# Kernel tuning notes

Measured on AMD Instinct MI355X. Metric: run time of the kernel, lower is better.

## Reference

```python
import jax, jax.numpy as jnp
import numpy as np

BN_EPS = 1e-5

def _bn_relu(x, gamma, beta):
    # BatchNorm1d in training mode: batch stats over (B, N) per channel
    mean = jnp.mean(x, axis=(0, 1), keepdims=True)
    var = jnp.var(x, axis=(0, 1), keepdims=True)
    return jax.nn.relu((x - mean) * jax.lax.rsqrt(var + BN_EPS) * gamma + beta)

def setup_inputs() -> dict:
    key = jax.random.key(0)
    ks = jax.random.split(key, 8)
    B, N, S, C1, C2 = 8, 8192, 2048, 128, 256
    return {
        'xyz1': jax.random.normal(ks[0], (B, N, 3), jnp.float32),
        'xyz2': jax.random.normal(ks[1], (B, S, 3), jnp.float32),
        'points1': jax.random.normal(ks[2], (B, N, C1), jnp.float32),
        'points2': jax.random.normal(ks[3], (B, S, C2), jnp.float32),
        'w0': jax.random.normal(ks[4], (256, C1 + C2), jnp.float32) * 0.02,
        'b0': jnp.zeros((256,), jnp.float32),
        'g0': jnp.ones((256,), jnp.float32),
        'be0': jnp.zeros((256,), jnp.float32),
        'w1': jax.random.normal(ks[5], (128, 256), jnp.float32) * 0.02,
        'b1': jnp.zeros((128,), jnp.float32),
        'g1': jnp.ones((128,), jnp.float32),
        'be1': jnp.zeros((128,), jnp.float32),
    }

def reference(xyz1, xyz2, points1, points2, w0, b0, g0, be0, w1, b1, g1, be1):
    # squared pairwise distances [B, N, S]
    sq = (jnp.sum(xyz1 * xyz1, -1)[:, :, None]
          - 2.0 * jnp.einsum('bnc,bmc->bnm', xyz1, xyz2)
          + jnp.sum(xyz2 * xyz2, -1)[:, None, :])
    neg_d, idx = jax.lax.top_k(-sq, 3)          # smallest 3 distances
    dist = -neg_d                               # [B, N, 3]
    recip = 1.0 / (dist + 1e-8)
    weight = recip / jnp.sum(recip, -1, keepdims=True)
    gathered = jax.vmap(lambda p, i: p[i])(points2, idx)   # [B, N, 3, C2]
    interp = jnp.sum(gathered * weight[..., None], axis=2)  # [B, N, C2]
    x = jnp.concatenate([points1, interp], axis=-1)         # [B, N, C1+C2]
    x = _bn_relu(jnp.einsum('bnc,oc->bno', x, w0) + b0, g0, be0)
    x = _bn_relu(jnp.einsum('bnc,oc->bno', x, w1) + b1, g1, be1)
    return x
```

## Files before the change

kernel.cpp:

```cpp
#include <hip/hip_runtime.h>

#define B_  8
#define N_  8192
#define S_  2048
#define C1_ 128
#define C2_ 256
#define KA_ 384
#define H0_ 256
#define H1_ 128
#define R_  (B_ * N_)

typedef __bf16 bf16;
typedef __attribute__((ext_vector_type(2))) __bf16 bf16x2;
typedef __attribute__((ext_vector_type(4))) __bf16 bf16x4;
typedef __attribute__((ext_vector_type(8))) __bf16 bf16x8;
typedef __attribute__((ext_vector_type(4))) float f32x4;

__device__ __forceinline__ void gload_lds16(const void* g, void* l) {
    __builtin_amdgcn_global_load_lds(
        (const __attribute__((address_space(1))) void*)g,
        (__attribute__((address_space(3))) void*)l, 16, 0, 0);
}

__global__ void zero_kernel(float* __restrict__ p, int n) {
    int i = blockIdx.x * 256 + threadIdx.x;
    if (i < n) p[i] = 0.f;
}

__global__ __launch_bounds__(256) void cvt_kernel(const float* __restrict__ src,
                                                  bf16* __restrict__ dst, int n4) {
    int i = blockIdx.x * 256 + threadIdx.x;
    if (i < n4) {
        float4 v = *(const float4*)(src + (size_t)i * 4);
        bf16x4 o = { (bf16)v.x, (bf16)v.y, (bf16)v.z, (bf16)v.w };
        *(bf16x4*)(dst + (size_t)i * 4) = o;
    }
}

__global__ __launch_bounds__(256) void top3_kernel(
    const float* __restrict__ xyz1, const float* __restrict__ xyz2,
    int* __restrict__ out_idx, float* __restrict__ out_w)
{
    __shared__ float4 sc[S_];
    __shared__ float  md[64][4][3];
    __shared__ int    mi[64][4][3];

    int b = blockIdx.x >> 7;
    int ntile = blockIdx.x & 127;
    const float* src = xyz2 + (size_t)b * S_ * 3;
    for (int i = threadIdx.x; i < S_; i += 256) {
        float x = src[i * 3 + 0], y = src[i * 3 + 1], z = src[i * 3 + 2];
        float4 c; c.x = x; c.y = y; c.z = z; c.w = x * x + y * y + z * z;
        sc[i] = c;
    }
    __syncthreads();

    const int q  = threadIdx.x >> 2;
    const int sp = threadIdx.x & 3;
    const size_t row = (size_t)b * N_ + ntile * 64 + q;
    const float ax = -2.f * xyz1[row * 3 + 0];
    const float ay = -2.f * xyz1[row * 3 + 1];
    const float az = -2.f * xyz1[row * 3 + 2];

    float m0 = 1e30f, m1 = 1e30f, m2 = 1e30f;
    int   j0 = 0, j1 = 0, j2 = 0;

    #pragma unroll 4
    for (int i = 0; i < S_ / 4; ++i) {
        int s = i * 4 + sp;
        float4 c = sc[s];
        float m = fmaf(ax, c.x, fmaf(ay, c.y, fmaf(az, c.z, c.w)));
        if (m < m2) {
            if (m < m1) {
                m2 = m1; j2 = j1;
                if (m < m0) { m1 = m0; j1 = j0; m0 = m; j0 = s; }
                else        { m1 = m;  j1 = s; }
            } else { m2 = m; j2 = s; }
        }
    }
    md[q][sp][0] = m0; md[q][sp][1] = m1; md[q][sp][2] = m2;
    mi[q][sp][0] = j0; mi[q][sp][1] = j1; mi[q][sp][2] = j2;
    __syncthreads();

    if (threadIdx.x < 64) {
        int qq = threadIdx.x;
        float d0 = md[qq][0][0], d1 = md[qq][0][1], d2 = md[qq][0][2];
        int   i0 = mi[qq][0][0], i1 = mi[qq][0][1], i2 = mi[qq][0][2];
        #pragma unroll
        for (int p = 1; p < 4; ++p) {
            #pragma unroll
            for (int j = 0; j < 3; ++j) {
                float d = md[qq][p][j]; int s = mi[qq][p][j];
                bool lt2 = (d < d2) || (d == d2 && s < i2);
                if (lt2) {
                    bool lt1 = (d < d1) || (d == d1 && s < i1);
                    if (lt1) {
                        d2 = d1; i2 = i1;
                        bool lt0 = (d < d0) || (d == d0 && s < i0);
                        if (lt0) { d1 = d0; i1 = i0; d0 = d; i0 = s; }
                        else     { d1 = d;  i1 = s; }
                    } else { d2 = d; i2 = s; }
                }
            }
        }
        size_t orow = (size_t)b * N_ + ntile * 64 + qq;
        float px = xyz1[orow * 3 + 0], py = xyz1[orow * 3 + 1], pz = xyz1[orow * 3 + 2];
        float pp = px * px + py * py + pz * pz;
        float r0 = 1.f / (d0 + pp + 1e-8f);
        float r1 = 1.f / (d1 + pp + 1e-8f);
        float r2 = 1.f / (d2 + pp + 1e-8f);
        float inv = 1.f / (r0 + r1 + r2);
        out_idx[orow * 3 + 0] = i0; out_idx[orow * 3 + 1] = i1; out_idx[orow * 3 + 2] = i2;
        out_w[orow * 3 + 0] = r0 * inv; out_w[orow * 3 + 1] = r1 * inv; out_w[orow * 3 + 2] = r2 * inv;
    }
}

__global__ __launch_bounds__(256) void interp_kernel(
    const float* __restrict__ points1, const float* __restrict__ points2,
    const int* __restrict__ idx3, const float* __restrict__ w3,
    bf16* __restrict__ Abf)
{
    int t = threadIdx.x;
    size_t row = (size_t)blockIdx.x * 4 + (t >> 6);
    int lane = t & 63;
    int b = (int)(row >> 13);
    const float* p2 = points2 + (size_t)b * S_ * C2_;
    int ia = idx3[row * 3 + 0], ib = idx3[row * 3 + 1], ic = idx3[row * 3 + 2];
    float wa = w3[row * 3 + 0], wb = w3[row * 3 + 1], wc = w3[row * 3 + 2];
    float4 va = *(const float4*)(p2 + (size_t)ia * C2_ + lane * 4);
    float4 vb = *(const float4*)(p2 + (size_t)ib * C2_ + lane * 4);
    float4 vc = *(const float4*)(p2 + (size_t)ic * C2_ + lane * 4);
    bf16x4 o = { (bf16)(wa * va.x + wb * vb.x + wc * vc.x),
                 (bf16)(wa * va.y + wb * vb.y + wc * vc.y),
                 (bf16)(wa * va.z + wb * vb.z + wc * vc.z),
                 (bf16)(wa * va.w + wb * vb.w + wc * vc.w) };
    *(bf16x4*)(Abf + row * KA_ + C1_ + lane * 4) = o;

    float2 p = *(const float2*)(points1 + row * C1_ + lane * 2);
    bf16x2 po = { (bf16)p.x, (bf16)p.y };
    *(bf16x2*)(Abf + row * KA_ + lane * 2) = po;
}

template<int K, int OT, bool OUTBF>
__global__ __launch_bounds__(256) void mfma_gemm_kernel(
    const bf16* __restrict__ A, const bf16* __restrict__ Wt, void* __restrict__ Cout,
    float* __restrict__ sums, float* __restrict__ sumsq)
{
    __shared__ bf16 As[128 * 32];
    __shared__ bf16 Bs[128 * 32];
    __shared__ float csum[128], csumsq[128];
    const int tid = threadIdx.x;
    const int lane = tid & 63, wave = tid >> 6;
    const int wr = wave >> 1, wc = wave & 1;
    const int r0 = blockIdx.x * 128, o0 = blockIdx.y * 128;

    f32x4 acc[4][4] = {};

    const int l15 = lane & 15, g = lane >> 4;
    const int slot = g ^ ((l15 >> 1) & 3);
    int a_off[4], b_off[4];
    #pragma unroll
    for (int m = 0; m < 4; ++m) a_off[m] = (wr * 64 + m * 16 + l15) * 32 + slot * 8;
    #pragma unroll
    for (int n = 0; n < 4; ++n) b_off[n] = (wc * 64 + n * 16 + l15) * 32 + slot * 8;

    const int c0 = tid, c1 = tid + 256;
    const int ar0 = c0 >> 2, ar1 = c1 >> 2;
    const int kb0 = ((c0 & 3) ^ ((ar0 >> 1) & 3)) * 8;
    const int kb1 = ((c1 & 3) ^ ((ar1 >> 1) & 3)) * 8;

    if (tid < 128) { csum[tid] = 0.f; csumsq[tid] = 0.f; }

    for (int k0 = 0; k0 < K; k0 += 32) {
        __syncthreads();
        gload_lds16(A  + (size_t)(r0 + ar0) * K + k0 + kb0, &As[c0 * 8]);
        gload_lds16(A  + (size_t)(r0 + ar1) * K + k0 + kb1, &As[c1 * 8]);
        gload_lds16(Wt + (size_t)(o0 + ar0) * K + k0 + kb0, &Bs[c0 * 8]);
        gload_lds16(Wt + (size_t)(o0 + ar1) * K + k0 + kb1, &Bs[c1 * 8]);
        __syncthreads();
        bf16x8 af[4], bfr[4];
        #pragma unroll
        for (int m = 0; m < 4; ++m) af[m]  = *(const bf16x8*)&As[a_off[m]];
        #pragma unroll
        for (int n = 0; n < 4; ++n) bfr[n] = *(const bf16x8*)&Bs[b_off[n]];
        #pragma unroll
        for (int m = 0; m < 4; ++m)
            #pragma unroll
            for (int n = 0; n < 4; ++n)
                acc[m][n] = __builtin_amdgcn_mfma_f32_16x16x32_bf16(af[m], bfr[n], acc[m][n], 0, 0, 0);
    }

    const int crow = r0 + wr * 64 + g * 4;
    const int ccol = o0 + wc * 64 + l15;
    #pragma unroll
    for (int m = 0; m < 4; ++m)
        #pragma unroll
        for (int n = 0; n < 4; ++n)
            #pragma unroll
            for (int j = 0; j < 4; ++j) {
                size_t off = (size_t)(crow + m * 16 + j) * OT + ccol + n * 16;
                if (OUTBF) ((bf16*)Cout)[off] = (bf16)acc[m][n][j];
                else       ((float*)Cout)[off] = acc[m][n][j];
            }

    #pragma unroll
    for (int n = 0; n < 4; ++n) {
        float s = 0.f, q = 0.f;
        #pragma unroll
        for (int m = 0; m < 4; ++m)
            #pragma unroll
            for (int j = 0; j < 4; ++j) {
                float v = acc[m][n][j];
                s += v; q = fmaf(v, v, q);
            }
        int col = wc * 64 + n * 16 + l15;
        atomicAdd(&csum[col], s);
        atomicAdd(&csumsq[col], q);
    }
    __syncthreads();
    if (tid < 128) {
        atomicAdd(&sums[o0 + tid], csum[tid]);
        atomicAdd(&sumsq[o0 + tid], csumsq[tid]);
    }
}

__global__ __launch_bounds__(256) void mfma_gemm2_kernel(
    const bf16* __restrict__ Ahp, const bf16* __restrict__ Wt,
    const float* __restrict__ scale, const float* __restrict__ shift,
    float* __restrict__ Cout, float* __restrict__ sums, float* __restrict__ sumsq)
{
    constexpr int K = H0_, OT = H1_;
    __shared__ bf16 As[128 * 32];
    __shared__ bf16 Bs[128 * 32];
    __shared__ float csum[128], csumsq[128];
    const int tid = threadIdx.x;
    const int lane = tid & 63, wave = tid >> 6;
    const int wr = wave >> 1, wc = wave & 1;
    const int r0 = blockIdx.x * 128, o0 = blockIdx.y * 128;

    f32x4 acc[4][4] = {};

    const int l15 = lane & 15, g = lane >> 4;
    const int slot = g ^ ((l15 >> 1) & 3);
    int a_off[4], b_off[4];
    #pragma unroll
    for (int m = 0; m < 4; ++m) a_off[m] = (wr * 64 + m * 16 + l15) * 32 + slot * 8;
    #pragma unroll
    for (int n = 0; n < 4; ++n) b_off[n] = (wc * 64 + n * 16 + l15) * 32 + slot * 8;

    const int c0 = tid, c1 = tid + 256;
    const int ar0 = c0 >> 2, ar1 = c1 >> 2;
    const int kb0 = ((c0 & 3) ^ ((ar0 >> 1) & 3)) * 8;
    const int kb1 = ((c1 & 3) ^ ((ar1 >> 1) & 3)) * 8;

    if (tid < 128) { csum[tid] = 0.f; csumsq[tid] = 0.f; }

    for (int k0 = 0; k0 < K; k0 += 32) {
        bf16x8 va0 = *(const bf16x8*)(Ahp + (size_t)(r0 + ar0) * K + k0 + kb0);
        bf16x8 va1 = *(const bf16x8*)(Ahp + (size_t)(r0 + ar1) * K + k0 + kb1);
        float s0a[8], h0a[8], s1a[8], h1a[8];
        *(float4*)&s0a[0] = *(const float4*)(scale + k0 + kb0);
        *(float4*)&s0a[4] = *(const float4*)(scale + k0 + kb0 + 4);
        *(float4*)&h0a[0] = *(const float4*)(shift + k0 + kb0);
        *(float4*)&h0a[4] = *(const float4*)(shift + k0 + kb0 + 4);
        *(float4*)&s1a[0] = *(const float4*)(scale + k0 + kb1);
        *(float4*)&s1a[4] = *(const float4*)(scale + k0 + kb1 + 4);
        *(float4*)&h1a[0] = *(const float4*)(shift + k0 + kb1);
        *(float4*)&h1a[4] = *(const float4*)(shift + k0 + kb1 + 4);
        bf16x8 ra0, ra1;
        #pragma unroll
        for (int j = 0; j < 8; ++j) {
            float f0 = fmaxf(0.f, fmaf((float)va0[j], s0a[j], h0a[j]));
            float f1 = fmaxf(0.f, fmaf((float)va1[j], s1a[j], h1a[j]));
            ra0[j] = (bf16)f0; ra1[j] = (bf16)f1;
        }
        __syncthreads();
        gload_lds16(Wt + (size_t)(o0 + ar0) * K + k0 + kb0, &Bs[c0 * 8]);
        gload_lds16(Wt + (size_t)(o0 + ar1) * K + k0 + kb1, &Bs[c1 * 8]);
        *(bf16x8*)&As[c0 * 8] = ra0;
        *(bf16x8*)&As[c1 * 8] = ra1;
        __syncthreads();
        bf16x8 af[4], bfr[4];
        #pragma unroll
        for (int m = 0; m < 4; ++m) af[m]  = *(const bf16x8*)&As[a_off[m]];
        #pragma unroll
        for (int n = 0; n < 4; ++n) bfr[n] = *(const bf16x8*)&Bs[b_off[n]];
        #pragma unroll
        for (int m = 0; m < 4; ++m)
            #pragma unroll
            for (int n = 0; n < 4; ++n)
                acc[m][n] = __builtin_amdgcn_mfma_f32_16x16x32_bf16(af[m], bfr[n], acc[m][n], 0, 0, 0);
    }

    const int crow = r0 + wr * 64 + g * 4;
    const int ccol = o0 + wc * 64 + l15;
    #pragma unroll
    for (int m = 0; m < 4; ++m)
        #pragma unroll
        for (int n = 0; n < 4; ++n)
            #pragma unroll
            for (int j = 0; j < 4; ++j)
                ((float*)Cout)[(size_t)(crow + m * 16 + j) * OT + ccol + n * 16] = acc[m][n][j];

    #pragma unroll
    for (int n = 0; n < 4; ++n) {
        float s = 0.f, q = 0.f;
        #pragma unroll
        for (int m = 0; m < 4; ++m)
            #pragma unroll
            for (int j = 0; j < 4; ++j) {
                float v = acc[m][n][j];
                s += v; q = fmaf(v, v, q);
            }
        int col = wc * 64 + n * 16 + l15;
        atomicAdd(&csum[col], s);
        atomicAdd(&csumsq[col], q);
    }
    __syncthreads();
    if (tid < 128) {
        atomicAdd(&sums[o0 + tid], csum[tid]);
        atomicAdd(&sumsq[o0 + tid], csumsq[tid]);
    }
}

__global__ void finalize_kernel(const float* __restrict__ sums, const float* __restrict__ sumsq,
                                const float* __restrict__ g, const float* __restrict__ be,
                                float* __restrict__ scale, float* __restrict__ shift, float invR)
{
    int c = threadIdx.x;
    float mean = sums[c] * invR;
    float var = sumsq[c] * invR - mean * mean;
    float s = g[c] * rsqrtf(var + 1e-5f);
    scale[c] = s;
    shift[c] = be[c] - mean * s;
}

__global__ __launch_bounds__(256) void bnrelu_kernel(float* __restrict__ X,
                                                     const float* __restrict__ scale,
                                                     const float* __restrict__ shift)
{
    size_t i = (size_t)blockIdx.x * 256 + threadIdx.x;
    float4 v = *(float4*)(X + i * 4);
    int c = (int)((i * 4) & (H1_ - 1));
    v.x = fmaxf(0.f, v.x * scale[c + 0] + shift[c + 0]);
    v.y = fmaxf(0.f, v.y * scale[c + 1] + shift[c + 1]);
    v.z = fmaxf(0.f, v.z * scale[c + 2] + shift[c + 2]);
    v.w = fmaxf(0.f, v.w * scale[c + 3] + shift[c + 3]);
    *(float4*)(X + i * 4) = v;
}

extern "C" void kernel_launch(void* const* d_in, const int* in_sizes, int n_in,
                              void* d_out, int out_size, void* d_ws, size_t ws_size,
                              hipStream_t stream)
{
    const float* xyz1    = (const float*)d_in[0];
    const float* xyz2    = (const float*)d_in[1];
    const float* points1 = (const float*)d_in[2];
    const float* points2 = (const float*)d_in[3];
    const float* w0  = (const float*)d_in[4];
    const float* g0  = (const float*)d_in[6];
    const float* be0 = (const float*)d_in[7];
    const float* w1  = (const float*)d_in[8];
    const float* g1  = (const float*)d_in[10];
    const float* be1 = (const float*)d_in[11];
    float* out = (float*)d_out;
    char* ws = (char*)d_ws;

    bf16* Abf     = (bf16*)(ws);
    bf16* hpre_bf = (bf16*)(ws + 50331648);
    bf16* Wbf0    = (bf16*)(ws + 117440512);
    bf16* Wbf1    = (bf16*)(ws + 117637120);
    int*  idx3    = (int*) (ws + 117702656);
    float* w3     = (float*)(ws + 118489088);
    float* stats  = (float*)(ws + 119275520);
    float* sums0 = stats,        *sumsq0 = stats + 256;
    float* sums1 = stats + 512,  *sumsq1 = stats + 640;
    float* scale0 = stats + 768,  *shift0 = stats + 1024;
    float* scale1 = stats + 1280, *shift1 = stats + 1408;

    zero_kernel<<<3, 256, 0, stream>>>(stats, 768);
    cvt_kernel<<<96, 256, 0, stream>>>(w0, Wbf0, H0_ * KA_ / 4);
    cvt_kernel<<<32, 256, 0, stream>>>(w1, Wbf1, H1_ * H0_ / 4);
    top3_kernel<<<B_ * (N_ / 64), 256, 0, stream>>>(xyz1, xyz2, idx3, w3);
    interp_kernel<<<R_ / 4, 256, 0, stream>>>(points1, points2, idx3, w3, Abf);

    mfma_gemm_kernel<KA_, H0_, true><<<dim3(R_ / 128, 2), 256, 0, stream>>>(
        Abf, Wbf0, hpre_bf, sums0, sumsq0);
    finalize_kernel<<<1, 256, 0, stream>>>(sums0, sumsq0, g0, be0, scale0, shift0, 1.f / R_);

    mfma_gemm2_kernel<<<dim3(R_ / 128, 1), 256, 0, stream>>>(
        hpre_bf, Wbf1, scale0, shift0, out, sums1, sumsq1);
    finalize_kernel<<<1, 128, 0, stream>>>(sums1, sumsq1, g1, be1, scale1, shift1, 1.f / R_);
    bnrelu_kernel<<<R_ * H1_ / 4 / 256, 256, 0, stream>>>(out, scale1, shift1);
}
```

Baseline: 183.9 us.

## Fuse top3 with interpolation and fold BN finalize into consumer kernels

Merges the zero and weight-conversion launches into one prep kernel. Fuses top-3 search with the interpolation gather so indices and weights stay in shared memory instead of a global round trip. Computes the BN scale and shift inside gemm2 and bnrelu, removing both finalize launches, and makes bnrelu process four float4s per thread. Launch overhead and small global traffic drop, but the interpolation phase now runs inside the top3 grid with only 1024 blocks, which may reduce gather parallelism.

```diff
diff --git a/kernel.cpp b/kernel.cpp
--- a/kernel.cpp
+++ b/kernel.cpp
@@ -22,28 +22,39 @@
         (__attribute__((address_space(3))) void*)l, 16, 0, 0);
 }
 
-__global__ void zero_kernel(float* __restrict__ p, int n) {
-    int i = blockIdx.x * 256 + threadIdx.x;
-    if (i < n) p[i] = 0.f;
-}
-
-__global__ __launch_bounds__(256) void cvt_kernel(const float* __restrict__ src,
-                                                  bf16* __restrict__ dst, int n4) {
-    int i = blockIdx.x * 256 + threadIdx.x;
-    if (i < n4) {
-        float4 v = *(const float4*)(src + (size_t)i * 4);
+__global__ __launch_bounds__(256) void prep_kernel(const float* __restrict__ w0,
+                                                   const float* __restrict__ w1,
+                                                   bf16* __restrict__ Wbf0,
+                                                   bf16* __restrict__ Wbf1,
+                                                   float* __restrict__ stats)
+{
+    int blk = blockIdx.x, tid = threadIdx.x;
+    if (blk < 96) {
+        int i = blk * 256 + tid;
+        float4 v = *(const float4*)(w0 + (size_t)i * 4);
         bf16x4 o = { (bf16)v.x, (bf16)v.y, (bf16)v.z, (bf16)v.w };
-        *(bf16x4*)(dst + (size_t)i * 4) = o;
-    }
-}
-
-__global__ __launch_bounds__(256) void top3_kernel(
+        *(bf16x4*)(Wbf0 + (size_t)i * 4) = o;
+    } else if (blk < 128) {
+        int i = (blk - 96) * 256 + tid;
+        float4 v = *(const float4*)(w1 + (size_t)i * 4);
+        bf16x4 o = { (bf16)v.x, (bf16)v.y, (bf16)v.z, (bf16)v.w };
+        *(bf16x4*)(Wbf1 + (size_t)i * 4) = o;
+    } else {
+        #pragma unroll
+        for (int k = 0; k < 3; ++k) stats[k * 256 + tid] = 0.f;
+    }
+}
+
+__global__ __launch_bounds__(256) void top3_interp_kernel(
     const float* __restrict__ xyz1, const float* __restrict__ xyz2,
-    int* __restrict__ out_idx, float* __restrict__ out_w)
+    const float* __restrict__ points1, const float* __restrict__ points2,
+    bf16* __restrict__ Abf)
 {
     __shared__ float4 sc[S_];
     __shared__ float  md[64][4][3];
     __shared__ int    mi[64][4][3];
+    __shared__ int    sidx[64][3];
+    __shared__ float  sw[64][3];
 
     int b = blockIdx.x >> 7;
     int ntile = blockIdx.x & 127;
@@ -110,35 +121,31 @@
         float r1 = 1.f / (d1 + pp + 1e-8f);
         float r2 = 1.f / (d2 + pp + 1e-8f);
         float inv = 1.f / (r0 + r1 + r2);
-        out_idx[orow * 3 + 0] = i0; out_idx[orow * 3 + 1] = i1; out_idx[orow * 3 + 2] = i2;
-        out_w[orow * 3 + 0] = r0 * inv; out_w[orow * 3 + 1] = r1 * inv; out_w[orow * 3 + 2] = r2 * inv;
-    }
-}
-
-__global__ __launch_bounds__(256) void interp_kernel(
-    const float* __restrict__ points1, const float* __restrict__ points2,
-    const int* __restrict__ idx3, const float* __restrict__ w3,
-    bf16* __restrict__ Abf)
-{
-    int t = threadIdx.x;
-    size_t row = (size_t)blockIdx.x * 4 + (t >> 6);
-    int lane = t & 63;
-    int b = (int)(row >> 13);
+        sidx[qq][0] = i0; sidx[qq][1] = i1; sidx[qq][2] = i2;
+        sw[qq][0] = r0 * inv; sw[qq][1] = r1 * inv; sw[qq][2] = r2 * inv;
+    }
+    __syncthreads();
+
+    const int wv = threadIdx.x >> 6, ln = threadIdx.x & 63;
+    const size_t rowbase = (size_t)b * N_ + ntile * 64;
     const float* p2 = points2 + (size_t)b * S_ * C2_;
-    int ia = idx3[row * 3 + 0], ib = idx3[row * 3 + 1], ic = idx3[row * 3 + 2];
-    float wa = w3[row * 3 + 0], wb = w3[row * 3 + 1], wc = w3[row * 3 + 2];
-    float4 va = *(const float4*)(p2 + (size_t)ia * C2_ + lane * 4);
-    float4 vb = *(const float4*)(p2 + (size_t)ib * C2_ + lane * 4);
-    float4 vc = *(const float4*)(p2 + (size_t)ic * C2_ + lane * 4);
-    bf16x4 o = { (bf16)(wa * va.x + wb * vb.x + wc * vc.x),
-                 (bf16)(wa * va.y + wb * vb.y + wc * vc.y),
-                 (bf16)(wa * va.z + wb * vb.z + wc * vc.z),
-                 (bf16)(wa * va.w + wb * vb.w + wc * vc.w) };
-    *(bf16x4*)(Abf + row * KA_ + C1_ + lane * 4) = o;
-
-    float2 p = *(const float2*)(points1 + row * C1_ + lane * 2);
-    bf16x2 po = { (bf16)p.x, (bf16)p.y };
-    *(bf16x2*)(Abf + row * KA_ + lane * 2) = po;
+    for (int r = wv; r < 64; r += 4) {
+        size_t orow = rowbase + r;
+        int ia = sidx[r][0], ib = sidx[r][1], ic = sidx[r][2];
+        float wa = sw[r][0], wb = sw[r][1], wc = sw[r][2];
+        float4 va = *(const float4*)(p2 + (size_t)ia * C2_ + ln * 4);
+        float4 vb = *(const float4*)(p2 + (size_t)ib * C2_ + ln * 4);
+        float4 vc = *(const float4*)(p2 + (size_t)ic * C2_ + ln * 4);
+        bf16x4 o = { (bf16)(wa * va.x + wb * vb.x + wc * vc.x),
+                     (bf16)(wa * va.y + wb * vb.y + wc * vc.y),
+                     (bf16)(wa * va.z + wb * vb.z + wc * vc.z),
+                     (bf16)(wa * va.w + wb * vb.w + wc * vc.w) };
+        *(bf16x4*)(Abf + orow * KA_ + C1_ + ln * 4) = o;
+
+        float2 p = *(const float2*)(points1 + orow * C1_ + ln * 2);
+        bf16x2 po = { (bf16)p.x, (bf16)p.y };
+        *(bf16x2*)(Abf + orow * KA_ + ln * 2) = po;
+    }
 }
 
 template<int K, int OT, bool OUTBF>
@@ -226,18 +233,31 @@
 
 __global__ __launch_bounds__(256) void mfma_gemm2_kernel(
     const bf16* __restrict__ Ahp, const bf16* __restrict__ Wt,
-    const float* __restrict__ scale, const float* __restrict__ shift,
+    const float* __restrict__ sums0, const float* __restrict__ sumsq0,
+    const float* __restrict__ g0, const float* __restrict__ be0,
     float* __restrict__ Cout, float* __restrict__ sums, float* __restrict__ sumsq)
 {
     constexpr int K = H0_, OT = H1_;
     __shared__ bf16 As[128 * 32];
     __shared__ bf16 Bs[128 * 32];
     __shared__ float csum[128], csumsq[128];
+    __shared__ float sscale[256], sshift[256];
     const int tid = threadIdx.x;
     const int lane = tid & 63, wave = tid >> 6;
     const int wr = wave >> 1, wc = wave & 1;
     const int r0 = blockIdx.x * 128, o0 = blockIdx.y * 128;
 
+    {
+        const float invR = 1.f / (float)R_;
+        float mean = sums0[tid] * invR;
+        float var = sumsq0[tid] * invR - mean * mean;
+        float sv = g0[tid] * rsqrtf(var + 1e-5f);
+        sscale[tid] = sv;
+        sshift[tid] = be0[tid] - mean * sv;
+    }
+    if (tid < 128) { csum[tid] = 0.f; csumsq[tid] = 0.f; }
+    __syncthreads();
+
     f32x4 acc[4][4] = {};
 
     const int l15 = lane & 15, g = lane >> 4;
@@ -253,20 +273,18 @@
     const int kb0 = ((c0 & 3) ^ ((ar0 >> 1) & 3)) * 8;
     const int kb1 = ((c1 & 3) ^ ((ar1 >> 1) & 3)) * 8;
 
-    if (tid < 128) { csum[tid] = 0.f; csumsq[tid] = 0.f; }
-
     for (int k0 = 0; k0 < K; k0 += 32) {
         bf16x8 va0 = *(const bf16x8*)(Ahp + (size_t)(r0 + ar0) * K + k0 + kb0);
         bf16x8 va1 = *(const bf16x8*)(Ahp + (size_t)(r0 + ar1) * K + k0 + kb1);
         float s0a[8], h0a[8], s1a[8], h1a[8];
-        *(float4*)&s0a[0] = *(const float4*)(scale + k0 + kb0);
-        *(float4*)&s0a[4] = *(const float4*)(scale + k0 + kb0 + 4);
-        *(float4*)&h0a[0] = *(const float4*)(shift + k0 + kb0);
-        *(float4*)&h0a[4] = *(const float4*)(shift + k0 + kb0 + 4);
-        *(float4*)&s1a[0] = *(const float4*)(scale + k0 + kb1);
-        *(float4*)&s1a[4] = *(const float4*)(scale + k0 + kb1 + 4);
-        *(float4*)&h1a[0] = *(const float4*)(shift + k0 + kb1);
-        *(float4*)&h1a[4] = *(const float4*)(shift + k0 + kb1 + 4);
+        *(float4*)&s0a[0] = *(const float4*)(&sscale[k0 + kb0]);
+        *(float4*)&s0a[4] = *(const float4*)(&sscale[k0 + kb0 + 4]);
+        *(float4*)&h0a[0] = *(const float4*)(&sshift[k0 + kb0]);
+        *(float4*)&h0a[4] = *(const float4*)(&sshift[k0 + kb0 + 4]);
+        *(float4*)&s1a[0] = *(const float4*)(&sscale[k0 + kb1]);
+        *(float4*)&s1a[4] = *(const float4*)(&sscale[k0 + kb1 + 4]);
+        *(float4*)&h1a[0] = *(const float4*)(&sshift[k0 + kb1]);
+        *(float4*)&h1a[4] = *(const float4*)(&sshift[k0 + kb1 + 4]);
         bf16x8 ra0, ra1;
         #pragma unroll
         for (int j = 0; j < 8; ++j) {
@@ -323,30 +341,34 @@
     }
 }
 
-__global__ void finalize_kernel(const float* __restrict__ sums, const float* __restrict__ sumsq,
-                                const float* __restrict__ g, const float* __restrict__ be,
-                                float* __restrict__ scale, float* __restrict__ shift, float invR)
-{
-    int c = threadIdx.x;
-    float mean = sums[c] * invR;
-    float var = sumsq[c] * invR - mean * mean;
-    float s = g[c] * rsqrtf(var + 1e-5f);
-    scale[c] = s;
-    shift[c] = be[c] - mean * s;
-}
-
-__global__ __launch_bounds__(256) void bnrelu_kernel(float* __restrict__ X,
-                                                     const float* __restrict__ scale,
-                                                     const float* __restrict__ shift)
-{
-    size_t i = (size_t)blockIdx.x * 256 + threadIdx.x;
-    float4 v = *(float4*)(X + i * 4);
-    int c = (int)((i * 4) & (H1_ - 1));
-    v.x = fmaxf(0.f, v.x * scale[c + 0] + shift[c + 0]);
-    v.y = fmaxf(0.f, v.y * scale[c + 1] + shift[c + 1]);
-    v.z = fmaxf(0.f, v.z * scale[c + 2] + shift[c + 2]);
-    v.w = fmaxf(0.f, v.w * scale[c + 3] + shift[c + 3]);
-    *(float4*)(X + i * 4) = v;
+__global__ __launch_bounds__(256) void bnrelu_kernel(
+    float* __restrict__ X, const float* __restrict__ sums1,
+    const float* __restrict__ sumsq1, const float* __restrict__ g1,
+    const float* __restrict__ be1)
+{
+    __shared__ float ss[128], sh[128];
+    int tid = threadIdx.x;
+    if (tid < 128) {
+        const float invR = 1.f / (float)R_;
+        float mean = sums1[tid] * invR;
+        float var = sumsq1[tid] * invR - mean * mean;
+        float sv = g1[tid] * rsqrtf(var + 1e-5f);
+        ss[tid] = sv;
+        sh[tid] = be1[tid] - mean * sv;
+    }
+    __syncthreads();
+
+    #pragma unroll
+    for (int it = 0; it < 4; ++it) {
+        size_t i = (size_t)it * 524288 + (size_t)blockIdx.x * 256 + tid;
+        int c = ((int)i & 31) * 4;
+        float4 v = *(float4*)(X + i * 4);
+        v.x = fmaxf(0.f, v.x * ss[c + 0] + sh[c + 0]);
+        v.y = fmaxf(0.f, v.y * ss[c + 1] + sh[c + 1]);
+        v.z = fmaxf(0.f, v.z * ss[c + 2] + sh[c + 2]);
+        v.w = fmaxf(0.f, v.w * ss[c + 3] + sh[c + 3]);
+        *(float4*)(X + i * 4) = v;
+    }
 }
 
 extern "C" void kernel_launch(void* const* d_in, const int* in_sizes, int n_in,
@@ -370,26 +392,18 @@
     bf16* hpre_bf = (bf16*)(ws + 50331648);
     bf16* Wbf0    = (bf16*)(ws + 117440512);
     bf16* Wbf1    = (bf16*)(ws + 117637120);
-    int*  idx3    = (int*) (ws + 117702656);
-    float* w3     = (float*)(ws + 118489088);
     float* stats  = (float*)(ws + 119275520);
     float* sums0 = stats,        *sumsq0 = stats + 256;
     float* sums1 = stats + 512,  *sumsq1 = stats + 640;
-    float* scale0 = stats + 768,  *shift0 = stats + 1024;
-    float* scale1 = stats + 1280, *shift1 = stats + 1408;
-
-    zero_kernel<<<3, 256, 0, stream>>>(stats, 768);
-    cvt_kernel<<<96, 256, 0, stream>>>(w0, Wbf0, H0_ * KA_ / 4);
-    cvt_kernel<<<32, 256, 0, stream>>>(w1, Wbf1, H1_ * H0_ / 4);
-    top3_kernel<<<B_ * (N_ / 64), 256, 0, stream>>>(xyz1, xyz2, idx3, w3);
-    interp_kernel<<<R_ / 4, 256, 0, stream>>>(points1, points2, idx3, w3, Abf);
+
+    prep_kernel<<<129, 256, 0, stream>>>(w0, w1, Wbf0, Wbf1, stats);
+    top3_interp_kernel<<<B_ * (N_ / 64), 256, 0, stream>>>(xyz1, xyz2, points1, points2, Abf);
 
     mfma_gemm_kernel<KA_, H0_, true><<<dim3(R_ / 128, 2), 256, 0, stream>>>(
         Abf, Wbf0, hpre_bf, sums0, sumsq0);
-    finalize_kernel<<<1, 256, 0, stream>>>(sums0, sumsq0, g0, be0, scale0, shift0, 1.f / R_);
 
     mfma_gemm2_kernel<<<dim3(R_ / 128, 1), 256, 0, stream>>>(
-        hpre_bf, Wbf1, scale0, shift0, out, sums1, sumsq1);
-    finalize_kernel<<<1, 128, 0, stream>>>(sums1, sumsq1, g1, be1, scale1, shift1, 1.f / R_);
-    bnrelu_kernel<<<R_ * H1_ / 4 / 256, 256, 0, stream>>>(out, scale1, shift1);
-}
+        hpre_bf, Wbf1, sums0, sumsq0, g0, be0, out, sums1, sumsq1);
+
+    bnrelu_kernel<<<2048, 256, 0, stream>>>(out, sums1, sumsq1, g1, be1);
+}
```

Result: faster. 175.0 us (-4.8%).
